# Kernel tuning notes

Measured on AMD Instinct MI355X. Metric: run time of the kernel, lower is better.

The kernel has to match this reference:

```python
import jax, jax.numpy as jnp
import numpy as np
from jax import lax

EPS = float(np.finfo(np.float64).eps)  # matches np.finfo(float).eps in torch module
C, K = 32, 128   # coarse_num, event_num
B, T, TP = 4, 512, 1024


def _fine_probs(cf_logits, ftc):
    # p(fine k | coarse c(k)) : softmax of logits restricted to each coarse group
    e = jnp.exp(cf_logits - jnp.max(cf_logits))            # [K]
    denom = jax.ops.segment_sum(e, ftc, num_segments=C)    # [C]
    return e / denom[ftc]                                  # [K]


def setup_inputs() -> dict:
    key = jax.random.key(0)
    ks = jax.random.split(key, 7)
    past_event = jax.random.randint(ks[0], (B, T), 0, C)                     # coarse ids of past events
    dt = jax.random.uniform(ks[1], (B, T), minval=0.0, maxval=0.1)
    past_time = jnp.cumsum(dt, axis=-1).astype(jnp.float32)                  # increasing event times
    horizon = float(T) * 0.05
    time_tensor = jax.random.uniform(ks[2], (B, TP), minval=0.0, maxval=horizon).astype(jnp.float32)
    mu = 0.1 * jax.random.normal(ks[3], (C,), dtype=jnp.float32)
    alpha = 0.1 * jax.random.normal(ks[4], (C, C), dtype=jnp.float32)
    delta = 0.1 * jax.random.normal(ks[5], (C, C), dtype=jnp.float32)
    cf_logits = 0.1 * jax.random.normal(ks[6], (K,), dtype=jnp.float32)
    ftc = jnp.arange(K) % C                                                   # fine -> coarse map
    return dict(past_event=past_event, past_time=past_time, time_tensor=time_tensor,
                mu=mu, alpha=alpha, delta=delta, cf_logits=cf_logits, ftc=ftc)


def reference(past_event, past_time, time_tensor, mu, alpha, delta, cf_logits, ftc):
    Bb, Tp = time_tensor.shape
    Cc = mu.shape[0]
    past_alpha = jax.nn.softplus(alpha)[past_event]          # [B,T,C]
    past_delta = jax.nn.softplus(delta)[past_event] + EPS    # [B,T,C]

    def step(acc, xs):
        pa_i, pd_i, pt_i = xs                                # [B,C],[B,C],[B]
        et = time_tensor - pt_i[:, None]                     # [B,Tp]
        use = (et > EPS).astype(acc.dtype)                   # causal mask
        etc = jnp.where(et < EPS, 0.0, et)
        effect = pa_i[:, None, :] * jnp.exp(-pd_i[:, None, :] * etc[:, :, None])  # [B,Tp,C]
        return acc + effect * use[:, :, None], None

    acc0 = jnp.zeros((Bb, Tp, Cc), dtype=time_tensor.dtype)
    acc, _ = lax.scan(step, acc0,
                      (past_alpha.transpose(1, 0, 2), past_delta.transpose(1, 0, 2), past_time.T))
    all_inten = acc + jax.nn.softplus(mu)[None, None, :]     # [B,Tp,C]
    fine_inten = all_inten[..., ftc] * _fine_probs(cf_logits, ftc)  # [B,Tp,K]
    return fine_inten
```

## Files before the change

kernel.cpp:

```cpp
#include <hip/hip_runtime.h>

#define BB   4
#define TT   512
#define TPN  1024
#define CC   32
#define KK   128
#define TP_PER_BLOCK 8
#define EPSF 2.220446049250313e-16f

__device__ __forceinline__ float softplus_f(float x) {
    return fmaxf(x, 0.f) + log1pf(__expf(-fabsf(x)));
}

__global__ __launch_bounds__(256) void GHP_31052613550343_kernel(
    const int*   __restrict__ past_event,
    const float* __restrict__ past_time,
    const float* __restrict__ time_tensor,
    const float* __restrict__ mu,
    const float* __restrict__ alpha,
    const float* __restrict__ delta,
    const float* __restrict__ cf_logits,
    const int*   __restrict__ ftc,
    float*       __restrict__ out)
{
    __shared__ float2 sad_s[CC * CC];
    __shared__ float  pt_s[TT];
    __shared__ int    pev_s[TT];
    __shared__ float  l_s[KK];
    __shared__ float  e_s[KK];
    __shared__ float  p_s[KK];
    __shared__ int    ftc_s[KK];
    __shared__ float  spmu_s[CC];
    __shared__ float  inten_s[TP_PER_BLOCK][CC + 1];

    const int tid = threadIdx.x;
    const int blocks_per_b = TPN / TP_PER_BLOCK;
    const int b   = blockIdx.x / blocks_per_b;
    const int tp0 = (blockIdx.x % blocks_per_b) * TP_PER_BLOCK;

    for (int idx = tid; idx < CC * CC; idx += 256) {
        float a = softplus_f(alpha[idx]);
        float d = softplus_f(delta[idx]) + EPSF;
        sad_s[idx] = make_float2(a, d);
    }
    for (int i = tid; i < TT; i += 256) {
        pev_s[i] = past_event[b * TT + i];
        pt_s[i]  = past_time[b * TT + i];
    }
    if (tid < KK) { l_s[tid] = cf_logits[tid]; ftc_s[tid] = ftc[tid]; }
    if (tid < CC) { spmu_s[tid] = softplus_f(mu[tid]); }
    __syncthreads();

    if (tid < KK) {
        float mx = -1e30f;
        for (int j = 0; j < KK; ++j) mx = fmaxf(mx, l_s[j]);
        e_s[tid] = __expf(l_s[tid] - mx);
    }
    __syncthreads();
    if (tid < KK) {
        const int myc = ftc_s[tid];
        float den = 0.f;
        for (int j = 0; j < KK; ++j) den += (ftc_s[j] == myc) ? e_s[j] : 0.f;
        p_s[tid] = e_s[tid] / den;
    }

    const int c   = tid & (CC - 1);
    const int tpl = tid >> 5;
    const int tp  = tp0 + tpl;
    const float t = time_tensor[b * TPN + tp];

    int lo = 0, hi = TT;
    while (lo < hi) {
        int mid = (lo + hi) >> 1;
        if (t - pt_s[mid] > EPSF) lo = mid + 1; else hi = mid;
    }
    const int n = lo;

    float acc0 = 0.f, acc1 = 0.f, acc2 = 0.f, acc3 = 0.f;
    int i = 0;
    for (; i + 4 <= n; i += 4) {
        const float2 ad0 = sad_s[pev_s[i + 0] * CC + c];
        const float2 ad1 = sad_s[pev_s[i + 1] * CC + c];
        const float2 ad2 = sad_s[pev_s[i + 2] * CC + c];
        const float2 ad3 = sad_s[pev_s[i + 3] * CC + c];
        const float et0 = t - pt_s[i + 0];
        const float et1 = t - pt_s[i + 1];
        const float et2 = t - pt_s[i + 2];
        const float et3 = t - pt_s[i + 3];
        acc0 += ad0.x * __expf(-ad0.y * et0);
        acc1 += ad1.x * __expf(-ad1.y * et1);
        acc2 += ad2.x * __expf(-ad2.y * et2);
        acc3 += ad3.x * __expf(-ad3.y * et3);
    }
    for (; i < n; ++i) {
        const float2 ad = sad_s[pev_s[i] * CC + c];
        const float et  = t - pt_s[i];
        acc0 += ad.x * __expf(-ad.y * et);
    }

    inten_s[tpl][c] = ((acc0 + acc1) + (acc2 + acc3)) + spmu_s[c];
    __syncthreads();

    float* outb = out + (size_t)(b * TPN + tp0) * KK;
    #pragma unroll
    for (int j = 0; j < KK / CC; ++j) {
        const int k = c + j * CC;
        outb[tpl * KK + k] = inten_s[tpl][ftc_s[k]] * p_s[k];
    }
}

extern "C" void kernel_launch(void* const* d_in, const int* in_sizes, int n_in,
                              void* d_out, int out_size, void* d_ws, size_t ws_size,
                              hipStream_t stream) {
    const int*   past_event  = (const int*)  d_in[0];
    const float* past_time   = (const float*)d_in[1];
    const float* time_tensor = (const float*)d_in[2];
    const float* mu          = (const float*)d_in[3];
    const float* alpha       = (const float*)d_in[4];
    const float* delta       = (const float*)d_in[5];
    const float* cf_logits   = (const float*)d_in[6];
    const int*   ftc         = (const int*)  d_in[7];
    float*       out         = (float*)d_out;

    const int grid = BB * (TPN / TP_PER_BLOCK);
    GHP_31052613550343_kernel<<<grid, 256, 0, stream>>>(
        past_event, past_time, time_tensor, mu, alpha, delta, cf_logits, ftc, out);
}
```

Baseline: 96.08 us.

## Split parameter prep into separate kernel and split past-event loop across four waves

Moves the softplus and fine-probability setup into a one-block prep kernel that writes to workspace, so each main block only copies precomputed tables. The main kernel now handles 2 time points per block, and each time point's 512 past events are split into 4 interleaved slices handled by different waves. Partial sums are combined through shared memory before the output is written. It also folds log2e into delta so exp2 can be used, and packs time with the pre-scaled event index into float2 for vectorized LDS reads. The cost is an extra kernel launch and a grid four times larger.

Measured after the change: 91.93 us. 1.05x faster.

```diff
diff --git a/kernel.cpp b/kernel.cpp
--- a/kernel.cpp
+++ b/kernel.cpp
@@ -5,107 +5,127 @@
 #define TPN  1024
 #define CC   32
 #define KK   128
-#define TP_PER_BLOCK 8
 #define EPSF 2.220446049250313e-16f
+#define LOG2E 1.4426950408889634f
+
+#if __has_builtin(__builtin_amdgcn_exp2f)
+#define EXP2F(x) __builtin_amdgcn_exp2f(x)
+#else
+#define EXP2F(x) exp2f(x)
+#endif
 
 __device__ __forceinline__ float softplus_f(float x) {
     return fmaxf(x, 0.f) + log1pf(__expf(-fabsf(x)));
 }
 
-__global__ __launch_bounds__(256) void GHP_31052613550343_kernel(
+__global__ __launch_bounds__(256) void GHP_prep(
+    const float* __restrict__ mu, const float* __restrict__ alpha,
+    const float* __restrict__ delta, const float* __restrict__ cf_logits,
+    const int* __restrict__ ftc, float2* __restrict__ ws2)
+{
+    const int tid = threadIdx.x;
+    for (int idx = tid; idx < CC * CC; idx += 256) {
+        float a = softplus_f(alpha[idx]);
+        float d = (softplus_f(delta[idx]) + EPSF) * LOG2E;
+        ws2[idx] = make_float2(a, d);
+    }
+    if (tid < KK) {
+        float mx = -1e30f;
+        for (int j = 0; j < KK; ++j) mx = fmaxf(mx, cf_logits[j]);
+        const int myc = ftc[tid];
+        const float e = __expf(cf_logits[tid] - mx);
+        float den = 0.f;
+        for (int j = 0; j < KK; ++j) {
+            float ej = __expf(cf_logits[j] - mx);
+            den += (ftc[j] == myc) ? ej : 0.f;
+        }
+        const float p = e / den;
+        ws2[CC * CC + tid] = make_float2(p, softplus_f(mu[myc]) * p);
+    }
+}
+
+__global__ __launch_bounds__(256, 8) void GHP_main(
     const int*   __restrict__ past_event,
     const float* __restrict__ past_time,
     const float* __restrict__ time_tensor,
-    const float* __restrict__ mu,
-    const float* __restrict__ alpha,
-    const float* __restrict__ delta,
-    const float* __restrict__ cf_logits,
     const int*   __restrict__ ftc,
+    const float2* __restrict__ ws2,
     float*       __restrict__ out)
 {
-    __shared__ float2 sad_s[CC * CC];
-    __shared__ float  pt_s[TT];
-    __shared__ int    pev_s[TT];
-    __shared__ float  l_s[KK];
-    __shared__ float  e_s[KK];
-    __shared__ float  p_s[KK];
-    __shared__ int    ftc_s[KK];
-    __shared__ float  spmu_s[CC];
-    __shared__ float  inten_s[TP_PER_BLOCK][CC + 1];
+    __shared__ __align__(16) float2 sad_s[CC * CC];
+    __shared__ __align__(16) float2 ptev_s[4 * 128];
+    __shared__ __align__(16) float2 pk_s[KK];
+    __shared__ int   ftc_s[KK];
+    __shared__ float part_s[2 * 4 * CC];
 
     const int tid = threadIdx.x;
-    const int blocks_per_b = TPN / TP_PER_BLOCK;
-    const int b   = blockIdx.x / blocks_per_b;
-    const int tp0 = (blockIdx.x % blocks_per_b) * TP_PER_BLOCK;
+    const int b   = blockIdx.x >> 9;
+    const int tp0 = (blockIdx.x & 511) << 1;
 
-    for (int idx = tid; idx < CC * CC; idx += 256) {
-        float a = softplus_f(alpha[idx]);
-        float d = softplus_f(delta[idx]) + EPSF;
-        sad_s[idx] = make_float2(a, d);
+    {
+        const float4* src = (const float4*)ws2;
+        float4* dst = (float4*)sad_s;
+        dst[tid]       = src[tid];
+        dst[tid + 256] = src[tid + 256];
     }
+    if (tid < 64) ((float4*)pk_s)[tid] = ((const float4*)(ws2 + CC * CC))[tid];
+    if (tid < KK) ftc_s[tid] = ftc[tid];
     for (int i = tid; i < TT; i += 256) {
-        pev_s[i] = past_event[b * TT + i];
-        pt_s[i]  = past_time[b * TT + i];
+        const int r = i & 3, j = i >> 2;
+        ptev_s[(r << 7) + j] = make_float2(past_time[b * TT + i],
+                                           __int_as_float(past_event[b * TT + i] << 5));
     }
-    if (tid < KK) { l_s[tid] = cf_logits[tid]; ftc_s[tid] = ftc[tid]; }
-    if (tid < CC) { spmu_s[tid] = softplus_f(mu[tid]); }
     __syncthreads();
 
-    if (tid < KK) {
-        float mx = -1e30f;
-        for (int j = 0; j < KK; ++j) mx = fmaxf(mx, l_s[j]);
-        e_s[tid] = __expf(l_s[tid] - mx);
+    const int c   = tid & 31;
+    const int h   = (tid >> 5) & 1;
+    const int w   = (tid >> 6) & 1;
+    const int tpl = tid >> 7;
+    const int r   = (w << 1) + h;
+    const float t = time_tensor[b * TPN + tp0 + tpl];
+
+    const float2* pp = ptev_s + (r << 7);
+    int lo = 0, hi = 128;
+    #pragma unroll
+    for (int s = 0; s < 8; ++s) {
+        const int mid = (lo + hi) >> 1;
+        const bool go = (lo < hi) && ((t - pp[mid].x) > EPSF);
+        lo = go ? mid + 1 : lo;
+        hi = go ? hi : mid;
     }
-    __syncthreads();
-    if (tid < KK) {
-        const int myc = ftc_s[tid];
-        float den = 0.f;
-        for (int j = 0; j < KK; ++j) den += (ftc_s[j] == myc) ? e_s[j] : 0.f;
-        p_s[tid] = e_s[tid] / den;
+    const int J = lo;
+
+    float acc0 = 0.f, acc1 = 0.f;
+    int j = 0;
+    #pragma unroll 2
+    for (; j + 4 <= J; j += 4) {
+        const float4 q0 = *(const float4*)(pp + j);
+        const float4 q1 = *(const float4*)(pp + j + 2);
+        const float2 ad0 = sad_s[__float_as_int(q0.y) + c];
+        const float2 ad1 = sad_s[__float_as_int(q0.w) + c];
+        const float2 ad2 = sad_s[__float_as_int(q1.y) + c];
+        const float2 ad3 = sad_s[__float_as_int(q1.w) + c];
+        acc0 = fmaf(ad0.x, EXP2F(-ad0.y * (t - q0.x)), acc0);
+        acc1 = fmaf(ad1.x, EXP2F(-ad1.y * (t - q0.z)), acc1);
+        acc0 = fmaf(ad2.x, EXP2F(-ad2.y * (t - q1.x)), acc0);
+        acc1 = fmaf(ad3.x, EXP2F(-ad3.y * (t - q1.z)), acc1);
     }
-
-    const int c   = tid & (CC - 1);
-    const int tpl = tid >> 5;
-    const int tp  = tp0 + tpl;
-    const float t = time_tensor[b * TPN + tp];
-
-    int lo = 0, hi = TT;
-    while (lo < hi) {
-        int mid = (lo + hi) >> 1;
-        if (t - pt_s[mid] > EPSF) lo = mid + 1; else hi = mid;
+    for (; j < J; ++j) {
+        const float2 pe = pp[j];
+        const float2 ad = sad_s[__float_as_int(pe.y) + c];
+        acc0 = fmaf(ad.x, EXP2F(-ad.y * (t - pe.x)), acc0);
     }
-    const int n = lo;
-
-    float acc0 = 0.f, acc1 = 0.f, acc2 = 0.f, acc3 = 0.f;
-    int i = 0;
-    for (; i + 4 <= n; i += 4) {
-        const float2 ad0 = sad_s[pev_s[i + 0] * CC + c];
-        const float2 ad1 = sad_s[pev_s[i + 1] * CC + c];
-        const float2 ad2 = sad_s[pev_s[i + 2] * CC + c];
-        const float2 ad3 = sad_s[pev_s[i + 3] * CC + c];
-        const float et0 = t - pt_s[i + 0];
-        const float et1 = t - pt_s[i + 1];
-        const float et2 = t - pt_s[i + 2];
-        const float et3 = t - pt_s[i + 3];
-        acc0 += ad0.x * __expf(-ad0.y * et0);
-        acc1 += ad1.x * __expf(-ad1.y * et1);
-        acc2 += ad2.x * __expf(-ad2.y * et2);
-        acc3 += ad3.x * __expf(-ad3.y * et3);
-    }
-    for (; i < n; ++i) {
-        const float2 ad = sad_s[pev_s[i] * CC + c];
-        const float et  = t - pt_s[i];
-        acc0 += ad.x * __expf(-ad.y * et);
-    }
-
-    inten_s[tpl][c] = ((acc0 + acc1) + (acc2 + acc3)) + spmu_s[c];
+    part_s[((tpl << 2) + r) * CC + c] = acc0 + acc1;
     __syncthreads();
 
-    float* outb = out + (size_t)(b * TPN + tp0) * KK;
-    #pragma unroll
-    for (int j = 0; j < KK / CC; ++j) {
-        const int k = c + j * CC;
-        outb[tpl * KK + k] = inten_s[tpl][ftc_s[k]] * p_s[k];
+    {
+        const int k   = tid & 127;
+        const int tpe = tid >> 7;
+        const int ck  = ftc_s[k];
+        const float* ps = part_s + (tpe << 7);
+        const float inten = (ps[ck] + ps[CC + ck]) + (ps[2 * CC + ck] + ps[3 * CC + ck]);
+        const float2 pv = pk_s[k];
+        out[(size_t)(b * TPN + tp0 + tpe) * KK + k] = fmaf(inten, pv.x, pv.y);
     }
 }
 
@@ -121,8 +141,9 @@
     const float* cf_logits   = (const float*)d_in[6];
     const int*   ftc         = (const int*)  d_in[7];
     float*       out         = (float*)d_out;
+    float2*      ws2         = (float2*)d_ws;
 
-    const int grid = BB * (TPN / TP_PER_BLOCK);
-    GHP_31052613550343_kernel<<<grid, 256, 0, stream>>>(
-        past_event, past_time, time_tensor, mu, alpha, delta, cf_logits, ftc, out);
+    GHP_prep<<<1, 256, 0, stream>>>(mu, alpha, delta, cf_logits, ftc, ws2);
+    GHP_main<<<BB * (TPN / 2), 256, 0, stream>>>(past_event, past_time, time_tensor,
+                                                 ftc, ws2, out);
 }
```
